# Kernel tuning notes

Measured on AMD Instinct MI355X. Metric: run time of the kernel, lower is better.

The kernel has to match this reference:

```python
import jax, jax.numpy as jnp
import numpy as np

N = 100000
E = 1600000
G = 128


def _degrees(src, dst, n):
    ones = jnp.ones(src.shape[0], dtype=jnp.float32)
    deg_out = jax.ops.segment_sum(ones, src, num_segments=n)
    deg_in = jax.ops.segment_sum(ones, dst, num_segments=n)
    return jnp.maximum(deg_out, 1.0), jnp.maximum(deg_in, 1.0)


def gcn_conv(x, W, b, src, dst, norm_out, norm_in):
    # DGL GraphConv, norm='both': scale src by d_out^-1/2, sum over edges,
    # scale dst by d_in^-1/2, then linear. Weight applied first (out<=in) --
    # mathematically identical, cheaper gather.
    h = (x * norm_out[:, None]) @ W          # [N, out]
    m = h[src]                               # [E, out] gather
    agg = jax.ops.segment_sum(m, dst, num_segments=N)  # [N, out] scatter-add
    return agg * norm_in[:, None] + b


def setup_inputs() -> dict:
    key = jax.random.key(0)
    ks = jax.random.split(key, 8)
    x = jax.random.normal(ks[0], (N, 128), dtype=jnp.float32)
    W1 = jax.random.normal(ks[1], (128, 64), dtype=jnp.float32) * (1.0 / np.sqrt(128))
    b1 = jnp.zeros((64,), dtype=jnp.float32)
    W2 = jax.random.normal(ks[2], (64, 16), dtype=jnp.float32) * (1.0 / np.sqrt(64))
    b2 = jnp.zeros((16,), dtype=jnp.float32)
    src = jax.random.randint(ks[3], (E,), 0, N, dtype=jnp.int32)
    dst = jax.random.randint(ks[4], (E,), 0, N, dtype=jnp.int32)
    graph_ids = jnp.sort(jax.random.randint(ks[5], (N,), 0, G, dtype=jnp.int32))
    return {"x": x, "W1": W1, "b1": b1, "W2": W2, "b2": b2,
            "src": src, "dst": dst, "graph_ids": graph_ids}


def reference(x, W1, b1, W2, b2, src, dst, graph_ids):
    deg_out, deg_in = _degrees(src, dst, N)
    norm_out = jax.lax.rsqrt(deg_out)
    norm_in = jax.lax.rsqrt(deg_in)
    h = gcn_conv(x, W1, b1, src, dst, norm_out, norm_in)
    h = jax.nn.relu(h)
    # dropout(p=0.2) is identity in eval mode
    h = gcn_conv(h, W2, b2, src, dst, norm_out, norm_in)
    # dgl.mean_nodes: per-graph mean pooling
    sums = jax.ops.segment_sum(h, graph_ids, num_segments=G)      # [G, 16]
    counts = jax.ops.segment_sum(jnp.ones((N,), jnp.float32), graph_ids, num_segments=G)
    return sums / jnp.maximum(counts, 1.0)[:, None]
```

## Files before the change

### kernel.cpp

```cpp
#include <hip/hip_runtime.h>
#include <hip/hip_fp16.h>

#define N_NODES 100000
#define N_EDGES 1600000
#define N_GRAPHS 128
#define NBUCK 391
#define NBLK 250
#define CHUNK_E4 1600

typedef unsigned long long u64;
typedef unsigned int u32;
typedef unsigned char u8;

__global__ __launch_bounds__(256) void k_cnt(const int4* __restrict__ src4,
                                             const int4* __restrict__ dst4,
                                             int* __restrict__ counts_d,
                                             int* __restrict__ counts_s) {
  __shared__ int hd[NBUCK], hs[NBUCK];
  const int t = threadIdx.x, blk = blockIdx.x;
  for (int j = t; j < NBUCK; j += 256) { hd[j] = 0; hs[j] = 0; }
  __syncthreads();
  const int start = blk * CHUNK_E4, end = start + CHUNK_E4;
  for (int i = start + t; i < end; i += 256) {
    int4 d = dst4[i]; int4 s = src4[i];
    atomicAdd(&hd[d.x >> 8], 1); atomicAdd(&hd[d.y >> 8], 1);
    atomicAdd(&hd[d.z >> 8], 1); atomicAdd(&hd[d.w >> 8], 1);
    atomicAdd(&hs[s.x >> 8], 1); atomicAdd(&hs[s.y >> 8], 1);
    atomicAdd(&hs[s.z >> 8], 1); atomicAdd(&hs[s.w >> 8], 1);
  }
  __syncthreads();
  for (int j = t; j < NBUCK; j += 256) {
    counts_d[j * NBLK + blk] = hd[j];
    counts_s[j * NBLK + blk] = hs[j];
  }
}

__global__ __launch_bounds__(256) void k_scanA(int* __restrict__ counts_d,
                                               int* __restrict__ counts_s,
                                               int* __restrict__ totals_d,
                                               int* __restrict__ totals_s) {
  __shared__ int s[256];
  const int b = blockIdx.x, t = threadIdx.x;
  int v = (t < NBLK) ? counts_d[b * NBLK + t] : 0;
  s[t] = v;
  __syncthreads();
  for (int off = 1; off < 256; off <<= 1) {
    int a = (t >= off) ? s[t - off] : 0;
    __syncthreads(); s[t] += a; __syncthreads();
  }
  if (t < NBLK) counts_d[b * NBLK + t] = s[t] - v;
  if (t == 255) totals_d[b] = s[t];
  __syncthreads();
  v = (t < NBLK) ? counts_s[b * NBLK + t] : 0;
  s[t] = v;
  __syncthreads();
  for (int off = 1; off < 256; off <<= 1) {
    int a = (t >= off) ? s[t - off] : 0;
    __syncthreads(); s[t] += a; __syncthreads();
  }
  if (t < NBLK) counts_s[b * NBLK + t] = s[t] - v;
  if (t == 255) totals_s[b] = s[t];
}

__global__ __launch_bounds__(512) void k_scanB(const int* __restrict__ totals_d,
                                               const int* __restrict__ totals_s,
                                               int* __restrict__ boff_d,
                                               int* __restrict__ boff_s,
                                               int* __restrict__ row_ptr) {
  __shared__ int s[512];
  const int t = threadIdx.x;
  int v = (t < NBUCK) ? totals_d[t] : 0;
  s[t] = v;
  __syncthreads();
  for (int off = 1; off < 512; off <<= 1) {
    int a = (t >= off) ? s[t - off] : 0;
    __syncthreads(); s[t] += a; __syncthreads();
  }
  if (t < NBUCK) boff_d[t] = s[t] - v;
  if (t == 0) { boff_d[NBUCK] = N_EDGES; row_ptr[N_NODES] = N_EDGES; }
  __syncthreads();
  v = (t < NBUCK) ? totals_s[t] : 0;
  s[t] = v;
  __syncthreads();
  for (int off = 1; off < 512; off <<= 1) {
    int a = (t >= off) ? s[t - off] : 0;
    __syncthreads(); s[t] += a; __syncthreads();
  }
  if (t < NBUCK) boff_s[t] = s[t] - v;
  if (t == 0) boff_s[NBUCK] = N_EDGES;
}

__global__ __launch_bounds__(256) void k_scatter(const int4* __restrict__ src4,
                                                 const int4* __restrict__ dst4,
                                                 const int* __restrict__ counts_d,
                                                 const int* __restrict__ counts_s,
                                                 const int* __restrict__ boff_d,
                                                 const int* __restrict__ boff_s,
                                                 u32* __restrict__ ed,
                                                 u8* __restrict__ ssk8) {
  __shared__ int cur_d[NBUCK], cur_s[NBUCK];
  const int t = threadIdx.x, blk = blockIdx.x;
  for (int j = t; j < NBUCK; j += 256) {
    cur_d[j] = boff_d[j] + counts_d[j * NBLK + blk];
    cur_s[j] = boff_s[j] + counts_s[j * NBLK + blk];
  }
  __syncthreads();
  const int start = blk * CHUNK_E4, end = start + CHUNK_E4;
  for (int i = start + t; i < end; i += 256) {
    int4 d4 = dst4[i]; int4 s4 = src4[i];
    {
      int d = d4.x, s = s4.x;
      int pd = atomicAdd(&cur_d[d >> 8], 1);
      ed[pd] = ((u32)(d & 255) << 24) | (u32)s;
      int ps = atomicAdd(&cur_s[s >> 8], 1);
      ssk8[ps] = (u8)(s & 255);
    }
    {
      int d = d4.y, s = s4.y;
      int pd = atomicAdd(&cur_d[d >> 8], 1);
      ed[pd] = ((u32)(d & 255) << 24) | (u32)s;
      int ps = atomicAdd(&cur_s[s >> 8], 1);
      ssk8[ps] = (u8)(s & 255);
    }
    {
      int d = d4.z, s = s4.z;
      int pd = atomicAdd(&cur_d[d >> 8], 1);
      ed[pd] = ((u32)(d & 255) << 24) | (u32)s;
      int ps = atomicAdd(&cur_s[s >> 8], 1);
      ssk8[ps] = (u8)(s & 255);
    }
    {
      int d = d4.w, s = s4.w;
      int pd = atomicAdd(&cur_d[d >> 8], 1);
      ed[pd] = ((u32)(d & 255) << 24) | (u32)s;
      int ps = atomicAdd(&cur_s[s >> 8], 1);
      ssk8[ps] = (u8)(s & 255);
    }
  }
}

__global__ __launch_bounds__(256) void k_bucket_csr(const u32* __restrict__ ed,
                                                    const int* __restrict__ boff_d,
                                                    int* __restrict__ row_ptr,
                                                    float* __restrict__ norm_in,
                                                    int* __restrict__ edge_src) {
  __shared__ int hist[256], scanbuf[256], cursor[256];
  const int b = blockIdx.x, t = threadIdx.x;
  const int base = b << 8;
  const int lo = boff_d[b], hi = boff_d[b + 1];
  hist[t] = 0;
  __syncthreads();
  for (int i = lo + t; i < hi; i += 256)
    atomicAdd(&hist[ed[i] >> 24], 1);
  __syncthreads();
  int v = hist[t];
  scanbuf[t] = v;
  __syncthreads();
  for (int off = 1; off < 256; off <<= 1) {
    int a = (t >= off) ? scanbuf[t - off] : 0;
    __syncthreads(); scanbuf[t] += a; __syncthreads();
  }
  int excl = scanbuf[t] - v;
  int node = base + t;
  if (node < N_NODES) {
    row_ptr[node] = lo + excl;
    norm_in[node] = rsqrtf(fmaxf((float)v, 1.0f));
  }
  cursor[t] = excl;
  __syncthreads();
  for (int i = lo + t; i < hi; i += 256) {
    u32 e = ed[i];
    int p = atomicAdd(&cursor[e >> 24], 1);
    edge_src[lo + p] = (int)(e & 0x00FFFFFFu);
  }
}

__global__ __launch_bounds__(256) void k_outdeg(const u8* __restrict__ ssk8,
                                                const int* __restrict__ boff_s,
                                                float* __restrict__ norm_out) {
  __shared__ int hist[256];
  const int b = blockIdx.x, t = threadIdx.x;
  const int base = b << 8;
  const int lo = boff_s[b], hi = boff_s[b + 1];
  hist[t] = 0;
  __syncthreads();
  for (int i = lo + t; i < hi; i += 256)
    atomicAdd(&hist[ssk8[i]], 1);
  __syncthreads();
  int node = base + t;
  if (node < N_NODES)
    norm_out[node] = rsqrtf(fmaxf((float)hist[t], 1.0f));
}

__global__ __launch_bounds__(256) void k_gemm1(const float* __restrict__ x,
                                               const float* __restrict__ W1,
                                               const float* __restrict__ norm_out,
                                               __half* __restrict__ h1h) {
  __shared__ float Wt[128 * 64];
  __shared__ float xt[64 * 132];
  const int t = threadIdx.x;
  const int row0 = blockIdx.x * 64;

  const float4* W4 = (const float4*)W1;
  float4* Wt4 = (float4*)Wt;
  #pragma unroll
  for (int i = 0; i < 8; ++i) Wt4[t + 256 * i] = W4[t + 256 * i];

  const float4* x4 = (const float4*)x;
  #pragma unroll
  for (int i = 0; i < 8; ++i) {
    int idx = t + 256 * i;
    int r = idx >> 5;
    int c4 = idx & 31;
    int row = row0 + r;
    float4 v = make_float4(0.f, 0.f, 0.f, 0.f);
    if (row < N_NODES) {
      float s = norm_out[row];
      v = x4[(size_t)row * 32 + c4];
      v.x *= s; v.y *= s; v.z *= s; v.w *= s;
    }
    *(float4*)&xt[r * 132 + c4 * 4] = v;
  }
  __syncthreads();

  const int tc = (t & 15) * 4;
  const int tr = (t >> 4) * 4;
  float acc[4][4] = {{0.f}};
  for (int k = 0; k < 128; k += 4) {
    float4 xa[4], wb[4];
    #pragma unroll
    for (int i = 0; i < 4; ++i) xa[i] = *(const float4*)&xt[(tr + i) * 132 + k];
    #pragma unroll
    for (int j = 0; j < 4; ++j) wb[j] = *(const float4*)&Wt[(k + j) * 64 + tc];
    #pragma unroll
    for (int i = 0; i < 4; ++i) {
      const float* xp = (const float*)&xa[i];
      #pragma unroll
      for (int j = 0; j < 4; ++j) {
        const float* wp = (const float*)&wb[j];
        acc[i][0] += xp[j] * wp[0];
        acc[i][1] += xp[j] * wp[1];
        acc[i][2] += xp[j] * wp[2];
        acc[i][3] += xp[j] * wp[3];
      }
    }
  }
  #pragma unroll
  for (int i = 0; i < 4; ++i) {
    int row = row0 + tr + i;
    if (row < N_NODES) {
      __half2 p0 = __float22half2_rn(make_float2(acc[i][0], acc[i][1]));
      __half2 p1 = __float22half2_rn(make_float2(acc[i][2], acc[i][3]));
      uint2 pk = make_uint2(*(u32*)&p0, *(u32*)&p1);
      *(uint2*)(h1h + (size_t)row * 64 + tc) = pk;
    }
  }
}

__global__ __launch_bounds__(256) void k_gather_l1(const int* __restrict__ row_ptr,
                                                   const int* __restrict__ edge_src,
                                                   const __half* __restrict__ h1h,
                                                   const float* __restrict__ norm_in,
                                                   const float* __restrict__ norm_out,
                                                   const float* __restrict__ b1,
                                                   const float* __restrict__ W2,
                                                   __half* __restrict__ h2h) {
  __shared__ float W2s[64 * 17];
  const int t = threadIdx.x;
  for (int i = t; i < 64 * 16; i += 256) W2s[(i >> 4) * 17 + (i & 15)] = W2[i];
  __syncthreads();

  const int w = t >> 6;
  const int l = t & 63;
  const int n = blockIdx.x * 4 + w;
  const int half = l >> 5;
  const u32 c = (u32)(l & 31);

  const u32* __restrict__ h1u = (const u32*)h1h;
  const int lo = row_ptr[n], hi = row_ptr[n + 1];

  float2 a0 = {0.f,0.f}, a1 = {0.f,0.f}, a2 = {0.f,0.f}, a3 = {0.f,0.f};
  float2 a4 = {0.f,0.f}, a5 = {0.f,0.f}, a6 = {0.f,0.f}, a7 = {0.f,0.f};
  int i = lo;
  for (; i + 16 <= hi; i += 16) {
    int sv = edge_src[i + (l & 15)];
    int s0 = __shfl(sv,  0 + half, 64);
    int s1 = __shfl(sv,  2 + half, 64);
    int s2 = __shfl(sv,  4 + half, 64);
    int s3 = __shfl(sv,  6 + half, 64);
    int s4 = __shfl(sv,  8 + half, 64);
    int s5 = __shfl(sv, 10 + half, 64);
    int s6 = __shfl(sv, 12 + half, 64);
    int s7 = __shfl(sv, 14 + half, 64);
    u32 v0 = h1u[(u32)s0 * 32u + c];
    u32 v1 = h1u[(u32)s1 * 32u + c];
    u32 v2 = h1u[(u32)s2 * 32u + c];
    u32 v3 = h1u[(u32)s3 * 32u + c];
    u32 v4 = h1u[(u32)s4 * 32u + c];
    u32 v5 = h1u[(u32)s5 * 32u + c];
    u32 v6 = h1u[(u32)s6 * 32u + c];
    u32 v7 = h1u[(u32)s7 * 32u + c];
    float2 f;
    f = __half22float2(*(__half2*)&v0); a0.x += f.x; a0.y += f.y;
    f = __half22float2(*(__half2*)&v1); a1.x += f.x; a1.y += f.y;
    f = __half22float2(*(__half2*)&v2); a2.x += f.x; a2.y += f.y;
    f = __half22float2(*(__half2*)&v3); a3.x += f.x; a3.y += f.y;
    f = __half22float2(*(__half2*)&v4); a4.x += f.x; a4.y += f.y;
    f = __half22float2(*(__half2*)&v5); a5.x += f.x; a5.y += f.y;
    f = __half22float2(*(__half2*)&v6); a6.x += f.x; a6.y += f.y;
    f = __half22float2(*(__half2*)&v7); a7.x += f.x; a7.y += f.y;
  }
  if (i + 8 <= hi) {
    int sv = edge_src[i + (l & 7)];
    int s0 = __shfl(sv, 0 + half, 64);
    int s1 = __shfl(sv, 2 + half, 64);
    int s2 = __shfl(sv, 4 + half, 64);
    int s3 = __shfl(sv, 6 + half, 64);
    u32 v0 = h1u[(u32)s0 * 32u + c];
    u32 v1 = h1u[(u32)s1 * 32u + c];
    u32 v2 = h1u[(u32)s2 * 32u + c];
    u32 v3 = h1u[(u32)s3 * 32u + c];
    float2 f;
    f = __half22float2(*(__half2*)&v0); a0.x += f.x; a0.y += f.y;
    f = __half22float2(*(__half2*)&v1); a1.x += f.x; a1.y += f.y;
    f = __half22float2(*(__half2*)&v2); a2.x += f.x; a2.y += f.y;
    f = __half22float2(*(__half2*)&v3); a3.x += f.x; a3.y += f.y;
    i += 8;
  }
  for (; i + 2 <= hi; i += 2) {
    int s = edge_src[i + half];
    u32 v = h1u[(u32)s * 32u + c];
    float2 f = __half22float2(*(__half2*)&v);
    a0.x += f.x; a0.y += f.y;
  }
  if (i < hi && half == 0) {
    int s = edge_src[i];
    u32 v = h1u[(u32)s * 32u + c];
    float2 f = __half22float2(*(__half2*)&v);
    a0.x += f.x; a0.y += f.y;
  }
  float accx = ((a0.x + a1.x) + (a2.x + a3.x)) + ((a4.x + a5.x) + (a6.x + a7.x));
  float accy = ((a0.y + a1.y) + (a2.y + a3.y)) + ((a4.y + a5.y) + (a6.y + a7.y));
  accx += __shfl_xor(accx, 32, 64);
  accy += __shfl_xor(accy, 32, 64);

  const float ni = norm_in[n];
  const float2 bb = ((const float2*)b1)[c];
  float h1x = fmaxf(accx * ni + bb.x, 0.0f);
  float h1y = fmaxf(accy * ni + bb.y, 0.0f);

  const int j = l & 15, p = l >> 4;
  float partial = 0.f;
  #pragma unroll
  for (int kk = 0; kk < 16; kk += 2) {
    int sl = p * 8 + (kk >> 1);
    float vx = __shfl(h1x, sl, 64);
    float vy = __shfl(h1y, sl, 64);
    partial += vx * W2s[(p * 16 + kk) * 17 + j];
    partial += vy * W2s[(p * 16 + kk + 1) * 17 + j];
  }
  partial += __shfl_xor(partial, 16, 64);
  partial += __shfl_xor(partial, 32, 64);
  if (l < 16) h2h[(size_t)n * 16 + l] = __float2half(norm_out[n] * partial);
}

__global__ __launch_bounds__(256) void k_gather_l2(const int* __restrict__ row_ptr,
                                                   const int* __restrict__ edge_src,
                                                   const __half* __restrict__ h2h,
                                                   const float* __restrict__ norm_in,
                                                   float* __restrict__ agg2) {
  const int t = threadIdx.x;
  const int w = t >> 6;
  const int l = t & 63;
  const int n = blockIdx.x * 4 + w;
  const int f2 = l & 7;
  const int p = l >> 3;

  const u32* __restrict__ h2u = (const u32*)h2h;
  const int lo = row_ptr[n], hi = row_ptr[n + 1];

  float ax = 0.f, ay = 0.f, bx = 0.f, by = 0.f;
  int i = lo + p;
  for (; i + 8 < hi; i += 16) {
    int s0 = edge_src[i], s1 = edge_src[i + 8];
    u32 v0 = h2u[(u32)s0 * 8u + (u32)f2];
    u32 v1 = h2u[(u32)s1 * 8u + (u32)f2];
    float2 g0 = __half22float2(*(__half2*)&v0);
    float2 g1 = __half22float2(*(__half2*)&v1);
    ax += g0.x; ay += g0.y;
    bx += g1.x; by += g1.y;
  }
  if (i < hi) {
    int s = edge_src[i];
    u32 v = h2u[(u32)s * 8u + (u32)f2];
    float2 g = __half22float2(*(__half2*)&v);
    ax += g.x; ay += g.y;
  }
  float sx = ax + bx, sy = ay + by;
  sx += __shfl_xor(sx, 8, 64);  sy += __shfl_xor(sy, 8, 64);
  sx += __shfl_xor(sx, 16, 64); sy += __shfl_xor(sy, 16, 64);
  sx += __shfl_xor(sx, 32, 64); sy += __shfl_xor(sy, 32, 64);
  if (l < 8) {
    float ni = norm_in[n];
    ((float2*)agg2)[(size_t)n * 8 + f2] = make_float2(sx * ni, sy * ni);
  }
}

__global__ __launch_bounds__(256) void k_pool(const float* __restrict__ agg2,
                                              const float* __restrict__ b2,
                                              const int* __restrict__ gid,
                                              float* __restrict__ out) {
  const int g = blockIdx.x;
  __shared__ int s_lo, s_hi;
  if (threadIdx.x == 0) {
    int a = 0, b = N_NODES;
    while (a < b) { int m = (a + b) >> 1; if (gid[m] < g) a = m + 1; else b = m; }
    s_lo = a;
    b = N_NODES;
    while (a < b) { int m = (a + b) >> 1; if (gid[m] < g + 1) a = m + 1; else b = m; }
    s_hi = a;
  }
  __syncthreads();
  const int lo = s_lo, hi = s_hi, cnt = hi - lo;
  const int j = threadIdx.x & 15;
  const int r = threadIdx.x >> 4;
  float acc = 0.f;
  for (int n = lo + r; n < hi; n += 16)
    acc += agg2[(size_t)n * 16 + j];

  __shared__ float red[256];
  red[threadIdx.x] = acc;
  __syncthreads();
  #pragma unroll
  for (int s = 8; s > 0; s >>= 1) {
    if (r < s) red[threadIdx.x] += red[threadIdx.x + s * 16];
    __syncthreads();
  }
  if (r == 0)
    out[g * 16 + j] = (cnt > 0) ? (red[j] / (float)cnt + b2[j]) : 0.0f;
}

extern "C" void kernel_launch(void* const* d_in, const int* in_sizes, int n_in,
                              void* d_out, int out_size, void* d_ws, size_t ws_size,
                              hipStream_t stream) {
  const float* x   = (const float*)d_in[0];
  const float* W1  = (const float*)d_in[1];
  const float* b1  = (const float*)d_in[2];
  const float* W2  = (const float*)d_in[3];
  const float* b2  = (const float*)d_in[4];
  const int*   src = (const int*)d_in[5];
  const int*   dst = (const int*)d_in[6];
  const int*   gid = (const int*)d_in[7];
  float* out = (float*)d_out;

  const size_t N = N_NODES, E = N_EDGES;
  float* wsf = (float*)d_ws;
  int*   wsi = (int*)d_ws;

  float* norm_out = wsf;
  float* norm_in  = wsf + N;
  int*   row_ptr  = wsi + 2 * N;
  int*   edge_src = wsi + 3 * N + 16;
  size_t S = 3 * N + 16 + E;
  u8*    ssk8     = (u8*)(wsi + S);
  int*   counts_d = wsi + S + E / 4;
  int*   counts_s = wsi + S + E / 4 + 97752;
  int*   totals_d = wsi + S + E / 4 + 195504;
  int*   totals_s = wsi + S + E / 4 + 195896;
  int*   boff_d   = wsi + S + E / 4 + 196288;
  int*   boff_s   = wsi + S + E / 4 + 196680;
  u32*   ed       = (u32*)(wsi + S + E / 4 + 197072);
  __half* h1h     = (__half*)(wsi + S);
  __half* h2h     = (__half*)(wsi + S + 32 * N);
  float*  agg2    = (float*)(wsi + S + 40 * N);

  const int4* src4 = (const int4*)src;
  const int4* dst4 = (const int4*)dst;

  k_cnt       <<<NBLK, 256, 0, stream>>>(src4, dst4, counts_d, counts_s);
  k_scanA     <<<NBUCK, 256, 0, stream>>>(counts_d, counts_s, totals_d, totals_s);
  k_scanB     <<<1, 512, 0, stream>>>(totals_d, totals_s, boff_d, boff_s, row_ptr);
  k_scatter   <<<NBLK, 256, 0, stream>>>(src4, dst4, counts_d, counts_s, boff_d, boff_s, ed, ssk8);
  k_bucket_csr<<<NBUCK, 256, 0, stream>>>(ed, boff_d, row_ptr, norm_in, edge_src);
  k_outdeg    <<<NBUCK, 256, 0, stream>>>(ssk8, boff_s, norm_out);
  k_gemm1     <<<(N_NODES + 63) / 64, 256, 0, stream>>>(x, W1, norm_out, h1h);
  k_gather_l1 <<<N_NODES / 4, 256, 0, stream>>>(row_ptr, edge_src, h1h, norm_in, norm_out, b1, W2, h2h);
  k_gather_l2 <<<N_NODES / 4, 256, 0, stream>>>(row_ptr, edge_src, h2h, norm_in, agg2);
  k_pool      <<<N_GRAPHS, 256, 0, stream>>>(agg2, b2, gid, out);
}
```

Measured before the change: 308.5 us.

## Use MFMA fp16 for first GEMM, fuse out-degree into CSR, pad gather tails

The first layer GEMM moves from scalar fp32 FMAs to fp16 MFMA 16x16x32 instructions, with x and W1 converted to fp16 in shared memory. The out-degree histogram kernel is merged into the bucket CSR kernel, which saves one launch. Both gather kernels drop their remainder loops and instead pad partial chunks with a sentinel zero row at index N_NODES. The gemm writes that extra row and gather_l1 zeroes it for layer 2. The cost is lower GEMM input precision and some wasted gathers on partial chunks.

Result: faster. 285.3 us (-7.5%).

```diff
diff --git a/kernel.cpp b/kernel.cpp
--- a/kernel.cpp
+++ b/kernel.cpp
@@ -7,10 +7,15 @@
 #define NBUCK 391
 #define NBLK 250
 #define CHUNK_E4 1600
+#define LDX 136
 
 typedef unsigned long long u64;
 typedef unsigned int u32;
 typedef unsigned char u8;
+typedef _Float16 f16;
+typedef f16 half8 __attribute__((ext_vector_type(8)));
+typedef f16 half4v __attribute__((ext_vector_type(4)));
+typedef float floatx4 __attribute__((ext_vector_type(4)));
 
 __global__ __launch_bounds__(256) void k_cnt(const int4* __restrict__ src4,
                                              const int4* __restrict__ dst4,
@@ -141,18 +146,27 @@
 
 __global__ __launch_bounds__(256) void k_bucket_csr(const u32* __restrict__ ed,
                                                     const int* __restrict__ boff_d,
+                                                    const u8* __restrict__ ssk8,
+                                                    const int* __restrict__ boff_s,
                                                     int* __restrict__ row_ptr,
                                                     float* __restrict__ norm_in,
+                                                    float* __restrict__ norm_out,
                                                     int* __restrict__ edge_src) {
-  __shared__ int hist[256], scanbuf[256], cursor[256];
+  __shared__ int hist[256], scanbuf[256], cursor[256], hist2[256];
   const int b = blockIdx.x, t = threadIdx.x;
   const int base = b << 8;
+  hist[t] = 0; hist2[t] = 0;
+  __syncthreads();
+  const int slo = boff_s[b], shi = boff_s[b + 1];
+  for (int i = slo + t; i < shi; i += 256)
+    atomicAdd(&hist2[ssk8[i]], 1);
   const int lo = boff_d[b], hi = boff_d[b + 1];
-  hist[t] = 0;
-  __syncthreads();
   for (int i = lo + t; i < hi; i += 256)
     atomicAdd(&hist[ed[i] >> 24], 1);
   __syncthreads();
+  int node = base + t;
+  if (node < N_NODES)
+    norm_out[node] = rsqrtf(fmaxf((float)hist2[t], 1.0f));
   int v = hist[t];
   scanbuf[t] = v;
   __syncthreads();
@@ -161,7 +175,6 @@
     __syncthreads(); scanbuf[t] += a; __syncthreads();
   }
   int excl = scanbuf[t] - v;
-  int node = base + t;
   if (node < N_NODES) {
     row_ptr[node] = lo + excl;
     norm_in[node] = rsqrtf(fmaxf((float)v, 1.0f));
@@ -175,43 +188,29 @@
   }
 }
 
-__global__ __launch_bounds__(256) void k_outdeg(const u8* __restrict__ ssk8,
-                                                const int* __restrict__ boff_s,
-                                                float* __restrict__ norm_out) {
-  __shared__ int hist[256];
-  const int b = blockIdx.x, t = threadIdx.x;
-  const int base = b << 8;
-  const int lo = boff_s[b], hi = boff_s[b + 1];
-  hist[t] = 0;
-  __syncthreads();
-  for (int i = lo + t; i < hi; i += 256)
-    atomicAdd(&hist[ssk8[i]], 1);
-  __syncthreads();
-  int node = base + t;
-  if (node < N_NODES)
-    norm_out[node] = rsqrtf(fmaxf((float)hist[t], 1.0f));
-}
-
 __global__ __launch_bounds__(256) void k_gemm1(const float* __restrict__ x,
                                                const float* __restrict__ W1,
                                                const float* __restrict__ norm_out,
                                                __half* __restrict__ h1h) {
-  __shared__ float Wt[128 * 64];
-  __shared__ float xt[64 * 132];
+  __shared__ __align__(16) f16 Xs[64 * LDX];
+  __shared__ __align__(16) f16 Ws[64 * LDX];
   const int t = threadIdx.x;
   const int row0 = blockIdx.x * 64;
 
   const float4* W4 = (const float4*)W1;
-  float4* Wt4 = (float4*)Wt;
-  #pragma unroll
-  for (int i = 0; i < 8; ++i) Wt4[t + 256 * i] = W4[t + 256 * i];
-
+  for (int i = t; i < 2048; i += 256) {
+    int k = i >> 4, n4 = (i & 15) * 4;
+    float4 v = W4[i];
+    Ws[(n4 + 0) * LDX + k] = (f16)v.x;
+    Ws[(n4 + 1) * LDX + k] = (f16)v.y;
+    Ws[(n4 + 2) * LDX + k] = (f16)v.z;
+    Ws[(n4 + 3) * LDX + k] = (f16)v.w;
+  }
   const float4* x4 = (const float4*)x;
   #pragma unroll
   for (int i = 0; i < 8; ++i) {
     int idx = t + 256 * i;
-    int r = idx >> 5;
-    int c4 = idx & 31;
+    int r = idx >> 5, c4 = idx & 31;
     int row = row0 + r;
     float4 v = make_float4(0.f, 0.f, 0.f, 0.f);
     if (row < N_NODES) {
@@ -219,40 +218,38 @@
       v = x4[(size_t)row * 32 + c4];
       v.x *= s; v.y *= s; v.z *= s; v.w *= s;
     }
-    *(float4*)&xt[r * 132 + c4 * 4] = v;
-  }
-  __syncthreads();
-
-  const int tc = (t & 15) * 4;
-  const int tr = (t >> 4) * 4;
-  float acc[4][4] = {{0.f}};
-  for (int k = 0; k < 128; k += 4) {
-    float4 xa[4], wb[4];
-    #pragma unroll
-    for (int i = 0; i < 4; ++i) xa[i] = *(const float4*)&xt[(tr + i) * 132 + k];
-    #pragma unroll
-    for (int j = 0; j < 4; ++j) wb[j] = *(const float4*)&Wt[(k + j) * 64 + tc];
-    #pragma unroll
-    for (int i = 0; i < 4; ++i) {
-      const float* xp = (const float*)&xa[i];
-      #pragma unroll
-      for (int j = 0; j < 4; ++j) {
-        const float* wp = (const float*)&wb[j];
-        acc[i][0] += xp[j] * wp[0];
-        acc[i][1] += xp[j] * wp[1];
-        acc[i][2] += xp[j] * wp[2];
-        acc[i][3] += xp[j] * wp[3];
-      }
-    }
-  }
+    half4v h = { (f16)v.x, (f16)v.y, (f16)v.z, (f16)v.w };
+    *(half4v*)&Xs[r * LDX + c4 * 4] = h;
+  }
+  __syncthreads();
+
+  const int w = t >> 6, l = t & 63;
+  const int m = l & 15, quad = l >> 4;
+  floatx4 c0 = {0.f,0.f,0.f,0.f}, c1 = {0.f,0.f,0.f,0.f};
+  floatx4 c2 = {0.f,0.f,0.f,0.f}, c3 = {0.f,0.f,0.f,0.f};
+  const f16* xrow = &Xs[(w * 16 + m) * LDX + quad * 8];
+  const f16* wrow = &Ws[m * LDX + quad * 8];
   #pragma unroll
-  for (int i = 0; i < 4; ++i) {
-    int row = row0 + tr + i;
-    if (row < N_NODES) {
-      __half2 p0 = __float22half2_rn(make_float2(acc[i][0], acc[i][1]));
-      __half2 p1 = __float22half2_rn(make_float2(acc[i][2], acc[i][3]));
-      uint2 pk = make_uint2(*(u32*)&p0, *(u32*)&p1);
-      *(uint2*)(h1h + (size_t)row * 64 + tc) = pk;
+  for (int kb = 0; kb < 4; ++kb) {
+    half8 a  = *(const half8*)(xrow + kb * 32);
+    half8 b0 = *(const half8*)(wrow + kb * 32);
+    half8 b1 = *(const half8*)(wrow + 16 * LDX + kb * 32);
+    half8 b2 = *(const half8*)(wrow + 32 * LDX + kb * 32);
+    half8 b3 = *(const half8*)(wrow + 48 * LDX + kb * 32);
+    c0 = __builtin_amdgcn_mfma_f32_16x16x32_f16(a, b0, c0, 0, 0, 0);
+    c1 = __builtin_amdgcn_mfma_f32_16x16x32_f16(a, b1, c1, 0, 0, 0);
+    c2 = __builtin_amdgcn_mfma_f32_16x16x32_f16(a, b2, c2, 0, 0, 0);
+    c3 = __builtin_amdgcn_mfma_f32_16x16x32_f16(a, b3, c3, 0, 0, 0);
+  }
+  #pragma unroll
+  for (int r = 0; r < 4; ++r) {
+    int row = row0 + w * 16 + quad * 4 + r;
+    if (row < N_NODES + 1) {
+      __half* dst = h1h + (size_t)row * 64 + m;
+      dst[0]  = __float2half(c0[r]);
+      dst[16] = __float2half(c1[r]);
+      dst[32] = __float2half(c2[r]);
+      dst[48] = __float2half(c3[r]);
     }
   }
 }
@@ -268,12 +265,13 @@
   __shared__ float W2s[64 * 17];
   const int t = threadIdx.x;
   for (int i = t; i < 64 * 16; i += 256) W2s[(i >> 4) * 17 + (i & 15)] = W2[i];
+  if (blockIdx.x == 0 && t < 16) h2h[(size_t)N_NODES * 16 + t] = __float2half(0.f);
   __syncthreads();
 
   const int w = t >> 6;
   const int l = t & 63;
   const int n = blockIdx.x * 4 + w;
-  const int half = l >> 5;
+  const int hf = l >> 5;
   const u32 c = (u32)(l & 31);
 
   const u32* __restrict__ h1u = (const u32*)h1h;
@@ -281,17 +279,17 @@
 
   float2 a0 = {0.f,0.f}, a1 = {0.f,0.f}, a2 = {0.f,0.f}, a3 = {0.f,0.f};
   float2 a4 = {0.f,0.f}, a5 = {0.f,0.f}, a6 = {0.f,0.f}, a7 = {0.f,0.f};
-  int i = lo;
-  for (; i + 16 <= hi; i += 16) {
-    int sv = edge_src[i + (l & 15)];
-    int s0 = __shfl(sv,  0 + half, 64);
-    int s1 = __shfl(sv,  2 + half, 64);
-    int s2 = __shfl(sv,  4 + half, 64);
-    int s3 = __shfl(sv,  6 + half, 64);
-    int s4 = __shfl(sv,  8 + half, 64);
-    int s5 = __shfl(sv, 10 + half, 64);
-    int s6 = __shfl(sv, 12 + half, 64);
-    int s7 = __shfl(sv, 14 + half, 64);
+  for (int i = lo; i < hi; i += 16) {
+    int idx = i + (l & 15);
+    int sv = (idx < hi) ? edge_src[idx] : (int)N_NODES;
+    int s0 = __shfl(sv,  0 + hf, 64);
+    int s1 = __shfl(sv,  2 + hf, 64);
+    int s2 = __shfl(sv,  4 + hf, 64);
+    int s3 = __shfl(sv,  6 + hf, 64);
+    int s4 = __shfl(sv,  8 + hf, 64);
+    int s5 = __shfl(sv, 10 + hf, 64);
+    int s6 = __shfl(sv, 12 + hf, 64);
+    int s7 = __shfl(sv, 14 + hf, 64);
     u32 v0 = h1u[(u32)s0 * 32u + c];
     u32 v1 = h1u[(u32)s1 * 32u + c];
     u32 v2 = h1u[(u32)s2 * 32u + c];
@@ -310,35 +308,6 @@
     f = __half22float2(*(__half2*)&v6); a6.x += f.x; a6.y += f.y;
     f = __half22float2(*(__half2*)&v7); a7.x += f.x; a7.y += f.y;
   }
-  if (i + 8 <= hi) {
-    int sv = edge_src[i + (l & 7)];
-    int s0 = __shfl(sv, 0 + half, 64);
-    int s1 = __shfl(sv, 2 + half, 64);
-    int s2 = __shfl(sv, 4 + half, 64);
-    int s3 = __shfl(sv, 6 + half, 64);
-    u32 v0 = h1u[(u32)s0 * 32u + c];
-    u32 v1 = h1u[(u32)s1 * 32u + c];
-    u32 v2 = h1u[(u32)s2 * 32u + c];
-    u32 v3 = h1u[(u32)s3 * 32u + c];
-    float2 f;
-    f = __half22float2(*(__half2*)&v0); a0.x += f.x; a0.y += f.y;
-    f = __half22float2(*(__half2*)&v1); a1.x += f.x; a1.y += f.y;
-    f = __half22float2(*(__half2*)&v2); a2.x += f.x; a2.y += f.y;
-    f = __half22float2(*(__half2*)&v3); a3.x += f.x; a3.y += f.y;
-    i += 8;
-  }
-  for (; i + 2 <= hi; i += 2) {
-    int s = edge_src[i + half];
-    u32 v = h1u[(u32)s * 32u + c];
-    float2 f = __half22float2(*(__half2*)&v);
-    a0.x += f.x; a0.y += f.y;
-  }
-  if (i < hi && half == 0) {
-    int s = edge_src[i];
-    u32 v = h1u[(u32)s * 32u + c];
-    float2 f = __half22float2(*(__half2*)&v);
-    a0.x += f.x; a0.y += f.y;
-  }
   float accx = ((a0.x + a1.x) + (a2.x + a3.x)) + ((a4.x + a5.x) + (a6.x + a7.x));
   float accy = ((a0.y + a1.y) + (a2.y + a3.y)) + ((a4.y + a5.y) + (a6.y + a7.y));
   accx += __shfl_xor(accx, 32, 64);
@@ -380,21 +349,16 @@
   const int lo = row_ptr[n], hi = row_ptr[n + 1];
 
   float ax = 0.f, ay = 0.f, bx = 0.f, by = 0.f;
-  int i = lo + p;
-  for (; i + 8 < hi; i += 16) {
-    int s0 = edge_src[i], s1 = edge_src[i + 8];
+  for (int base = lo; base < hi; base += 16) {
+    int i1 = base + p, i2 = base + p + 8;
+    int s0 = (i1 < hi) ? edge_src[i1] : (int)N_NODES;
+    int s1 = (i2 < hi) ? edge_src[i2] : (int)N_NODES;
     u32 v0 = h2u[(u32)s0 * 8u + (u32)f2];
     u32 v1 = h2u[(u32)s1 * 8u + (u32)f2];
     float2 g0 = __half22float2(*(__half2*)&v0);
     float2 g1 = __half22float2(*(__half2*)&v1);
     ax += g0.x; ay += g0.y;
     bx += g1.x; by += g1.y;
-  }
-  if (i < hi) {
-    int s = edge_src[i];
-    u32 v = h2u[(u32)s * 8u + (u32)f2];
-    float2 g = __half22float2(*(__half2*)&v);
-    ax += g.x; ay += g.y;
   }
   float sx = ax + bx, sy = ay + by;
   sx += __shfl_xor(sx, 8, 64);  sy += __shfl_xor(sy, 8, 64);
@@ -471,8 +435,8 @@
   int*   boff_s   = wsi + S + E / 4 + 196680;
   u32*   ed       = (u32*)(wsi + S + E / 4 + 197072);
   __half* h1h     = (__half*)(wsi + S);
-  __half* h2h     = (__half*)(wsi + S + 32 * N);
-  float*  agg2    = (float*)(wsi + S + 40 * N);
+  __half* h2h     = (__half*)(wsi + S + 32 * N + 40);
+  float*  agg2    = (float*)(wsi + S + 40 * N + 56);
 
   const int4* src4 = (const int4*)src;
   const int4* dst4 = (const int4*)dst;
@@ -481,9 +445,8 @@
   k_scanA     <<<NBUCK, 256, 0, stream>>>(counts_d, counts_s, totals_d, totals_s);
   k_scanB     <<<1, 512, 0, stream>>>(totals_d, totals_s, boff_d, boff_s, row_ptr);
   k_scatter   <<<NBLK, 256, 0, stream>>>(src4, dst4, counts_d, counts_s, boff_d, boff_s, ed, ssk8);
-  k_bucket_csr<<<NBUCK, 256, 0, stream>>>(ed, boff_d, row_ptr, norm_in, edge_src);
-  k_outdeg    <<<NBUCK, 256, 0, stream>>>(ssk8, boff_s, norm_out);
-  k_gemm1     <<<(N_NODES + 63) / 64, 256, 0, stream>>>(x, W1, norm_out, h1h);
+  k_bucket_csr<<<NBUCK, 256, 0, stream>>>(ed, boff_d, ssk8, boff_s, row_ptr, norm_in, norm_out, edge_src);
+  k_gemm1     <<<(N_NODES + 64) / 64, 256, 0, stream>>>(x, W1, norm_out, h1h);
   k_gather_l1 <<<N_NODES / 4, 256, 0, stream>>>(row_ptr, edge_src, h1h, norm_in, norm_out, b1, W2, h2h);
   k_gather_l2 <<<N_NODES / 4, 256, 0, stream>>>(row_ptr, edge_src, h2h, norm_in, agg2);
   k_pool      <<<N_GRAPHS, 256, 0, stream>>>(agg2, b2, gid, out);
```
